# Performance work log

Measured on AMD Instinct MI355X. Metric: run time of the kernel, lower is better.

Reference implementation:

```python
import jax, jax.numpy as jnp
import numpy as np

B, S, D = 4, 4096, 1024
H, F = 16, 256
HD = D // H  # 64


def setup_inputs() -> dict:
    key = jax.random.key(0)
    ks = jax.random.split(key, 10)
    scale = 1.0 / np.sqrt(D)
    x = jax.random.normal(ks[0], (B, S, D), dtype=jnp.float32)
    Wq = jax.random.normal(ks[1], (D, D), dtype=jnp.float32) * scale
    bq = jnp.zeros((D,), dtype=jnp.float32)
    Wk = jax.random.normal(ks[2], (D, D), dtype=jnp.float32) * scale
    bk = jnp.zeros((D,), dtype=jnp.float32)
    Wv = jax.random.normal(ks[3], (D, D), dtype=jnp.float32) * scale
    bv = jnp.zeros((D,), dtype=jnp.float32)
    Wo = jax.random.normal(ks[4], (D, D), dtype=jnp.float32) * scale
    bo = jnp.zeros((D,), dtype=jnp.float32)
    rf = jax.random.normal(ks[5], (H, HD, F), dtype=jnp.float32) / np.sqrt(F)
    return {"x": x, "Wq": Wq, "bq": bq, "Wk": Wk, "bk": bk,
            "Wv": Wv, "bv": bv, "Wo": Wo, "bo": bo, "rf": rf}


def _heads(y):
    # [B,S,D] -> [B,H,S,HD]
    return y.reshape(B, S, H, HD).transpose(0, 2, 1, 3)


def reference(x, Wq, bq, Wk, bk, Wv, bv, Wo, bo, rf):
    q = _heads(x @ Wq.T + bq)
    k = _heads(x @ Wk.T + bk)
    v = _heads(x @ Wv.T + bv)
    # positive feature maps: softplus(random projection)
    q_prime = jax.nn.softplus(jnp.einsum('bhsd,hdf->bhsf', q, rf))
    k_prime = jax.nn.softplus(jnp.einsum('bhsd,hdf->bhsf', k, rf))
    kv = jnp.einsum('bhsf,bhsd->bhfd', k_prime, v)          # [B,H,F,HD]
    k_sum = k_prime.sum(axis=2)                              # [B,H,F]
    qkv = jnp.einsum('bhsf,bhfd->bhsd', q_prime, kv)        # [B,H,S,HD]
    denom = jnp.einsum('bhsf,bhf->bhs', q_prime, k_sum) + 1e-8
    out = qkv / denom[..., None]
    out = out.transpose(0, 2, 1, 3).reshape(B, S, D)
    return out @ Wo.T + bo
```

## Files before the change

kernel.cpp:

```cpp
#include <hip/hip_runtime.h>
#include <hip/hip_bf16.h>
#include <math.h>

#define Bb 4
#define Ss 4096
#define Dd 1024
#define Hh 16
#define Ff 256
#define HDd 64
#define Mm (Bb*Ss)

typedef unsigned int u32;
typedef unsigned short u16;

typedef __attribute__((ext_vector_type(8))) short bf16x8;
typedef __attribute__((ext_vector_type(4))) float f32x4;

__device__ __forceinline__ float bflo(u32 u){ union{u32 i; float f;} c; c.i = u << 16; return c.f; }
__device__ __forceinline__ float bfhi(u32 u){ union{u32 i; float f;} c; c.i = u & 0xffff0000u; return c.f; }
__device__ __forceinline__ u16 f2b(float f){
  union{float f; u32 i;} c; c.f = f;
  u32 x = c.i;
  return (u16)((x + 0x7fffu + ((x >> 16) & 1u)) >> 16);
}
__device__ __forceinline__ u32 pk2(float lo, float hi){
  union { __hip_bfloat162 h; u32 u; } c;
  c.h = __float22bfloat162_rn(make_float2(lo, hi));
  return c.u;
}
__device__ __forceinline__ float sfast(float x){
  return fmaxf(x, 0.f) + __logf(1.f + __expf(-fabsf(x)));
}
__device__ __forceinline__ void gload_lds16(const u16* g, u16* l){
  __builtin_amdgcn_global_load_lds(
      (const __attribute__((address_space(1))) void*)g,
      (__attribute__((address_space(3))) void*)l, 16, 0, 0);
}

__global__ void cvt_bf16(const float* __restrict__ in, u16* __restrict__ out, int n)
{
  int i = (blockIdx.x * 256 + threadIdx.x) * 8;
  if (i >= n) return;
  float4 a = *reinterpret_cast<const float4*>(in + i);
  float4 b = *reinterpret_cast<const float4*>(in + i + 4);
  *reinterpret_cast<uint4*>(out + i) =
      make_uint4(pk2(a.x, a.y), pk2(a.z, a.w), pk2(b.x, b.y), pk2(b.z, b.w));
}

__global__ void cvt_w4(const float* __restrict__ w0, const float* __restrict__ w1,
                       const float* __restrict__ w2, const float* __restrict__ w3,
                       u16* __restrict__ out)
{
  const int y = blockIdx.y;
  const float* in = (y == 0) ? w0 : (y == 1) ? w1 : (y == 2) ? w2 : w3;
  int i = (blockIdx.x * 256 + threadIdx.x) * 8;
  float4 a = *reinterpret_cast<const float4*>(in + i);
  float4 b = *reinterpret_cast<const float4*>(in + i + 4);
  *reinterpret_cast<uint4*>(out + (size_t)y * Dd * Dd + i) =
      make_uint4(pk2(a.x, a.y), pk2(a.z, a.w), pk2(b.x, b.y), pk2(b.z, b.w));
}

__global__ void zero_f32(float* __restrict__ p, int n)
{
  int i = blockIdx.x * 256 + threadIdx.x;
  if (i < n) p[i] = 0.f;
}

template<typename OT, bool BROW>
__global__ __launch_bounds__(256, 2) void mfma_gemm_bt(
    const u16* __restrict__ A, const u16* __restrict__ W,
    const float* __restrict__ bias, OT* __restrict__ C,
    int M, int N, int K)
{
  __shared__ __align__(16) u16 As[128 * 64];
  __shared__ __align__(16) u16 Bs[128 * 64];

  const int tid = threadIdx.x;
  const int wave = tid >> 6, lane = tid & 63;
  const int quad = lane >> 4, lm = lane & 15;
  const int wm = (wave >> 1) * 64, wn = (wave & 1) * 64;
  const int m0 = blockIdx.x * 128, n0 = blockIdx.y * 128;

  int rr[4], cc4[4];
#pragma unroll
  for (int i = 0; i < 4; i++) {
    const int j = wave * 64 + i * 256 + lane;
    rr[i] = j >> 3;
    cc4[i] = (j & 7) ^ (rr[i] & 7);
  }

  f32x4 acc[4][4] = {};

  for (int k0 = 0; k0 < K; k0 += 64) {
#pragma unroll
    for (int i = 0; i < 4; i++) {
      u16* ldsA = &As[(wave * 64 + i * 256) * 8];
      u16* ldsB = &Bs[(wave * 64 + i * 256) * 8];
      gload_lds16(A + (size_t)(m0 + rr[i]) * K + k0 + cc4[i] * 8, ldsA);
      gload_lds16(W + (size_t)(n0 + rr[i]) * K + k0 + cc4[i] * 8, ldsB);
    }
    __syncthreads();

#pragma unroll
    for (int ks2 = 0; ks2 < 2; ks2++) {
      bf16x8 af[4], bf[4];
#pragma unroll
      for (int mi = 0; mi < 4; mi++) {
        const int row = wm + mi * 16 + lm;
        af[mi] = *reinterpret_cast<const bf16x8*>(
            &As[row * 64 + (((ks2 * 4 + quad) ^ (row & 7)) * 8)]);
      }
#pragma unroll
      for (int ni = 0; ni < 4; ni++) {
        const int row = wn + ni * 16 + lm;
        bf[ni] = *reinterpret_cast<const bf16x8*>(
            &Bs[row * 64 + (((ks2 * 4 + quad) ^ (row & 7)) * 8)]);
      }
#pragma unroll
      for (int mi = 0; mi < 4; mi++)
#pragma unroll
        for (int ni = 0; ni < 4; ni++)
          acc[mi][ni] = __builtin_amdgcn_mfma_f32_16x16x32_bf16(af[mi], bf[ni], acc[mi][ni], 0, 0, 0);
    }
    __syncthreads();
  }

#pragma unroll
  for (int mi = 0; mi < 4; mi++)
#pragma unroll
    for (int ni = 0; ni < 4; ni++) {
      const int n = n0 + wn + ni * 16 + lm;
      const float bvn = BROW ? 0.f : bias[n];
      const int mb = m0 + wm + mi * 16 + quad * 4;
      float v[4];
#pragma unroll
      for (int r = 0; r < 4; r++)
        v[r] = acc[mi][ni][r] + (BROW ? bias[mb + r] : bvn);
      if constexpr (sizeof(OT) == 2) {
        const u32 w01 = pk2(v[0], v[1]), w23 = pk2(v[2], v[3]);
        ((u16*)C)[(size_t)(mb + 0) * N + n] = (u16)w01;
        ((u16*)C)[(size_t)(mb + 1) * N + n] = (u16)(w01 >> 16);
        ((u16*)C)[(size_t)(mb + 2) * N + n] = (u16)w23;
        ((u16*)C)[(size_t)(mb + 3) * N + n] = (u16)(w23 >> 16);
      } else {
#pragma unroll
        for (int r = 0; r < 4; r++)
          ((float*)C)[(size_t)(mb + r) * N + n] = v[r];
      }
    }
}

__global__ void rf_transpose(const float* __restrict__ rf, float* __restrict__ rft)
{
  const int h = blockIdx.x, d = blockIdx.y, f = threadIdx.x;
  rft[((size_t)h * Ff + f) * HDd + d] = rf[((size_t)(h * HDd + d)) * Ff + f];
}

#define NSPLIT 16
#define SCHUNKS (Ss / NSPLIT / 64)

__global__ __launch_bounds__(256, 2) void kv_fused(
    const u16* __restrict__ Km, const u16* __restrict__ Vt,
    const float* __restrict__ rft, float* __restrict__ kv, float* __restrict__ ksum)
{
  __shared__ __align__(16) u16 KS[64 * 64];
  __shared__ __align__(16) u16 VS[64 * 64];
  __shared__ __align__(16) u16 PT[4][64 * 64];

  const int bh = blockIdx.x;
  const int b = bh >> 4, h = bh & 15;
  const int s0 = blockIdx.y * (Ss / NSPLIT);
  const int tid = threadIdx.x;
  const int wave = tid >> 6, lane = tid & 63;
  const int quad = lane >> 4, lm = lane & 15;
  const int F0 = wave * 64;

  bf16x8 bfr[4][2];
  {
    const float* rh = rft + (size_t)h * Ff * HDd;
#pragma unroll
    for (int ni = 0; ni < 4; ni++) {
      const float* rrow = rh + (size_t)(F0 + ni * 16 + lm) * HDd;
#pragma unroll
      for (int ks = 0; ks < 2; ks++) {
        float4 a = *reinterpret_cast<const float4*>(rrow + ks * 32 + quad * 8);
        float4 e = *reinterpret_cast<const float4*>(rrow + ks * 32 + quad * 8 + 4);
        union { u32 w[4]; bf16x8 v; } u;
        u.w[0] = pk2(a.x, a.y); u.w[1] = pk2(a.z, a.w);
        u.w[2] = pk2(e.x, e.y); u.w[3] = pk2(e.z, e.w);
        bfr[ni][ks] = u.v;
      }
    }
  }

  const int j0 = wave * 64 + lane, j1 = j0 + 256;
  const int r0 = j0 >> 3, c0 = (j0 & 7) ^ (r0 & 7);
  const int r1 = j1 >> 3, c1 = (j1 & 7) ^ (r1 & 7);

  f32x4 kvacc[4][4] = {};
  float kss[4] = {0.f, 0.f, 0.f, 0.f};

#pragma unroll 1
  for (int ch = 0; ch < SCHUNKS; ch++) {
    const int sc = s0 + ch * 64;
    gload_lds16(Km + (size_t)(b * Ss + sc + r0) * Dd + h * 64 + c0 * 8, &KS[(wave * 64) * 8]);
    gload_lds16(Km + (size_t)(b * Ss + sc + r1) * Dd + h * 64 + c1 * 8, &KS[(wave * 64 + 256) * 8]);
    gload_lds16(Vt + (size_t)(h * 64 + r0) * Mm + b * Ss + sc + c0 * 8, &VS[(wave * 64) * 8]);
    gload_lds16(Vt + (size_t)(h * 64 + r1) * Mm + b * Ss + sc + c1 * 8, &VS[(wave * 64 + 256) * 8]);
    __syncthreads();

#pragma unroll
    for (int mi = 0; mi < 4; mi++) {
      const int row = mi * 16 + lm;
      f32x4 pmi[4] = {};
#pragma unroll
      for (int ks2 = 0; ks2 < 2; ks2++) {
        bf16x8 af = *reinterpret_cast<const bf16x8*>(
            (const char*)KS + row * 128 + (((ks2 * 4 + quad) ^ (row & 7)) * 16));
#pragma unroll
        for (int ni = 0; ni < 4; ni++)
          pmi[ni] = __builtin_amdgcn_mfma_f32_16x16x32_bf16(af, bfr[ni][ks2], pmi[ni], 0, 0, 0);
      }
#pragma unroll
      for (int ni = 0; ni < 4; ni++) {
        float v0 = sfast(pmi[ni][0]);
        float v1 = sfast(pmi[ni][1]);
        float v2 = sfast(pmi[ni][2]);
        float v3 = sfast(pmi[ni][3]);
        kss[ni] += (v0 + v1) + (v2 + v3);
        int frow = ni * 16 + lm;
        int off = (frow * 128 + mi * 32 + quad * 8) ^ ((frow & 7) << 4);
        *reinterpret_cast<uint2*>((char*)&PT[wave][0] + off) =
            make_uint2(pk2(v0, v1), pk2(v2, v3));
      }
    }

#pragma unroll
    for (int ks2 = 0; ks2 < 2; ks2++) {
      bf16x8 a2[4], b2[4];
#pragma unroll
      for (int mi = 0; mi < 4; mi++) {
        int row = mi * 16 + lm;
        a2[mi] = *reinterpret_cast<const bf16x8*>(
            (char*)&PT[wave][0] + row * 128 + (((ks2 * 4 + quad) ^ (row & 7)) * 16));
      }
#pragma unroll
      for (int ni = 0; ni < 4; ni++) {
        int row = ni * 16 + lm;
        b2[ni] = *reinterpret_cast<const bf16x8*>(
            (const char*)VS + row * 128 + (((ks2 * 4 + quad) ^ (row & 7)) * 16));
      }
#pragma unroll
      for (int mi = 0; mi < 4; mi++)
#pragma unroll
        for (int ni = 0; ni < 4; ni++)
          kvacc[mi][ni] = __builtin_amdgcn_mfma_f32_16x16x32_bf16(a2[mi], b2[ni], kvacc[mi][ni], 0, 0, 0);
    }
    __syncthreads();
  }

  float* kvp = kv + (size_t)bh * Ff * HDd;
#pragma unroll
  for (int mi = 0; mi < 4; mi++)
#pragma unroll
    for (int ni = 0; ni < 4; ni++)
#pragma unroll
      for (int rr2 = 0; rr2 < 4; rr2++) {
        int f = F0 + mi * 16 + quad * 4 + rr2;
        int d = ni * 16 + lm;
        atomicAdd(kvp + (size_t)f * HDd + d, kvacc[mi][ni][rr2]);
      }
#pragma unroll
  for (int ni = 0; ni < 4; ni++) {
    float v = kss[ni];
    v += __shfl_xor(v, 16, 64);
    v += __shfl_xor(v, 32, 64);
    if (quad == 0) atomicAdd(ksum + (size_t)bh * Ff + F0 + ni * 16 + lm, v);
  }
}

__global__ void kvt_cvt(const float* __restrict__ kv, u16* __restrict__ kvtb)
{
  const int bh = blockIdx.x;
  const int d = threadIdx.x & 63, fg = threadIdx.x >> 6;
  const float* src = kv + (size_t)bh * Ff * HDd + d;
  u32* dst = reinterpret_cast<u32*>(kvtb + (size_t)bh * HDd * Ff + (size_t)d * Ff + fg * 64);
#pragma unroll
  for (int j = 0; j < 32; j++) {
    float v0 = src[(size_t)(fg * 64 + 2 * j) * HDd];
    float v1 = src[(size_t)(fg * 64 + 2 * j + 1) * HDd];
    dst[j] = pk2(v0, v1);
  }
}

#define ASPLIT 16
#define ACHUNKS (Ss / ASPLIT / 64)

__global__ __launch_bounds__(256, 2) void attn_fused(
    const u16* __restrict__ Qm, const float* __restrict__ rft,
    const u16* __restrict__ kvtb, const float* __restrict__ ksum,
    u16* __restrict__ attnb)
{
  __shared__ __align__(16) u16 P4[4][64 * 64];
  __shared__ __align__(16) float den4[64][4];

  const int bh = blockIdx.x;
  const int b = bh >> 4, h = bh & 15;
  const int s0 = blockIdx.y * (Ss / ASPLIT);
  const int tid = threadIdx.x;
  const int wave = tid >> 6, lane = tid & 63;
  const int quad = lane >> 4, lm = lane & 15;
  const int F0 = wave * 64;

  bf16x8 bfr[4][2];
  {
    const float* rh = rft + (size_t)h * Ff * HDd;
#pragma unroll
    for (int ni = 0; ni < 4; ni++) {
      const float* rrow = rh + (size_t)(F0 + ni * 16 + lm) * HDd;
#pragma unroll
      for (int ks = 0; ks < 2; ks++) {
        float4 a = *reinterpret_cast<const float4*>(rrow + ks * 32 + quad * 8);
        float4 e = *reinterpret_cast<const float4*>(rrow + ks * 32 + quad * 8 + 4);
        union { u32 w[4]; bf16x8 v; } u;
        u.w[0] = pk2(a.x, a.y); u.w[1] = pk2(a.z, a.w);
        u.w[2] = pk2(e.x, e.y); u.w[3] = pk2(e.z, e.w);
        bfr[ni][ks] = u.v;
      }
    }
  }
  bf16x8 b2r[4][2];
  {
    const u16* kb = kvtb + (size_t)bh * HDd * Ff + (size_t)(wave * 16 + lm) * Ff;
#pragma unroll
    for (int fb = 0; fb < 4; fb++)
#pragma unroll
      for (int k2 = 0; k2 < 2; k2++)
        b2r[fb][k2] = *reinterpret_cast<const bf16x8*>(kb + fb * 64 + k2 * 32 + quad * 8);
  }
  float ksv[4];
#pragma unroll
  for (int ni = 0; ni < 4; ni++)
    ksv[ni] = ksum[(size_t)bh * Ff + F0 + ni * 16 + lm];

  const int odd = lm & 1;
  u32 pOffA[4], pOffB[4];
  char* const ptb = (char*)&P4[wave][0];
  {
    const int ra = quad * 4 + (odd ? 2 : 0);
    const int rb = quad * 4 + (odd ? 3 : 1);
#pragma unroll
    for (int ni = 0; ni < 4; ni++) {
      const int fpb = ni * 16 + (lm & ~1);
      const int cc = fpb >> 3, bib = (fpb & 7) * 2;
      pOffA[ni] = ra * 128 + ((cc ^ (ra & 7)) << 4) + bib;
      pOffB[ni] = rb * 128 + ((cc ^ (rb & 7)) << 4) + bib;
    }
  }

  for (int ch = 0; ch < ACHUNKS; ch++) {
    const int sc0 = s0 + ch * 64;

    bf16x8 af[4][2];
#pragma unroll
    for (int mi = 0; mi < 4; mi++) {
      const u16* qrow = Qm + (size_t)(b * Ss + sc0 + mi * 16 + lm) * Dd + h * 64;
#pragma unroll
      for (int ks = 0; ks < 2; ks++)
        af[mi][ks] = *reinterpret_cast<const bf16x8*>(qrow + ks * 32 + quad * 8);
    }
    f32x4 p[4][4] = {};
#pragma unroll
    for (int ks = 0; ks < 2; ks++)
#pragma unroll
      for (int mi = 0; mi < 4; mi++)
#pragma unroll
        for (int ni = 0; ni < 4; ni++)
          p[mi][ni] = __builtin_amdgcn_mfma_f32_16x16x32_bf16(af[mi][ks], bfr[ni][ks], p[mi][ni], 0, 0, 0);

#pragma unroll
    for (int mi = 0; mi < 4; mi++) {
      const int sbase = mi * 16 + quad * 4;
      float dd[4] = {0.f, 0.f, 0.f, 0.f};
#pragma unroll
      for (int ni = 0; ni < 4; ni++) {
        u32 pk01 = pk2(sfast(p[mi][ni][0]), sfast(p[mi][ni][1]));
        u32 pk23 = pk2(sfast(p[mi][ni][2]), sfast(p[mi][ni][3]));
        dd[0] += bflo(pk01) * ksv[ni];
        dd[1] += bfhi(pk01) * ksv[ni];
        dd[2] += bflo(pk23) * ksv[ni];
        dd[3] += bfhi(pk23) * ksv[ni];
        u32 ob01 = (u32)__shfl_xor((int)pk01, 1, 64);
        u32 ob23 = (u32)__shfl_xor((int)pk23, 1, 64);
        u32 s0v = odd ? ob23 : pk01;
        u32 s1v = odd ? pk23 : ob01;
        u32 w_a = __builtin_amdgcn_perm(s1v, s0v, 0x05040100u);
        u32 w_b = __builtin_amdgcn_perm(s1v, s0v, 0x07060302u);
        *reinterpret_cast<u32*>(ptb + pOffA[ni] + mi * 2048) = w_a;
        *reinterpret_cast<u32*>(ptb + pOffB[ni] + mi * 2048) = w_b;
      }
#pragma unroll
      for (int r = 0; r < 4; r++) {
        float v = dd[r];
        v += __shfl_xor(v, 1, 64);
        v += __shfl_xor(v, 2, 64);
        v += __shfl_xor(v, 4, 64);
        v += __shfl_xor(v, 8, 64);
        if (lm == 0) den4[sbase + r][wave] = v;
      }
    }
    __syncthreads();

    f32x4 acc2[4] = {};
#pragma unroll
    for (int fb = 0; fb < 4; fb++)
#pragma unroll
      for (int k2 = 0; k2 < 2; k2++) {
        bf16x8 af2[4];
#pragma unroll
        for (int mi = 0; mi < 4; mi++) {
          int row = mi * 16 + lm;
          af2[mi] = *reinterpret_cast<const bf16x8*>(
              (char*)&P4[fb][0] + row * 128 + (((k2 * 4 + quad) ^ (row & 7)) << 4));
        }
#pragma unroll
        for (int mi = 0; mi < 4; mi++)
          acc2[mi] = __builtin_amdgcn_mfma_f32_16x16x32_bf16(af2[mi], b2r[fb][k2], acc2[mi], 0, 0, 0);
      }

#pragma unroll
    for (int mi = 0; mi < 4; mi++) {
      float o[4];
#pragma unroll
      for (int r = 0; r < 4; r++) {
        const int s = mi * 16 + quad * 4 + r;
        float4 dv = *reinterpret_cast<const float4*>(&den4[s][0]);
        const float inv = 1.f / ((dv.x + dv.y) + (dv.z + dv.w) + 1e-8f);
        o[r] = acc2[mi][r] * inv;
      }
      const u32 w01 = pk2(o[0], o[1]), w23 = pk2(o[2], o[3]);
      const size_t ob = (size_t)(b * Ss + sc0 + mi * 16 + quad * 4) * Dd + h * 64 + wave * 16 + lm;
      attnb[ob]          = (u16)w01;
      attnb[ob + Dd]     = (u16)(w01 >> 16);
      attnb[ob + 2 * Dd] = (u16)w23;
      attnb[ob + 3 * Dd] = (u16)(w23 >> 16);
    }
    __syncthreads();
  }
}

extern "C" void kernel_launch(void* const* d_in, const int* in_sizes, int n_in,
                              void* d_out, int out_size, void* d_ws, size_t ws_size,
                              hipStream_t stream)
{
  const float* x  = (const float*)d_in[0];
  const float* Wq = (const float*)d_in[1];
  const float* bq = (const float*)d_in[2];
  const float* Wk = (const float*)d_in[3];
  const float* bk = (const float*)d_in[4];
  const float* Wv = (const float*)d_in[5];
  const float* bv = (const float*)d_in[6];
  const float* Wo = (const float*)d_in[7];
  const float* bo = (const float*)d_in[8];
  const float* rf = (const float*)d_in[9];

  char* w = (char*)d_ws;
  u16* xb = (u16*)w;        w += (size_t)Mm * Dd * 2;
  u16* q  = (u16*)w;        w += (size_t)Mm * Dd * 2;
  u16* k  = (u16*)w;        w += (size_t)Mm * Dd * 2;
  u16* vt = (u16*)w;        w += (size_t)Mm * Dd * 2;
  u16* wqb = (u16*)w;       w += (size_t)Dd * Dd * 2;
  u16* wkb = (u16*)w;       w += (size_t)Dd * Dd * 2;
  u16* wvb = (u16*)w;       w += (size_t)Dd * Dd * 2;
  u16* wob = (u16*)w;       w += (size_t)Dd * Dd * 2;
  float* kv = (float*)w;    w += (size_t)(Bb * Hh) * Ff * HDd * 4;
  float* ks = (float*)w;    w += (size_t)(Bb * Hh) * Ff * 4;
  float* rft = (float*)w;   w += (size_t)Hh * Ff * HDd * 4;
  u16* kvtb = wqb;

  cvt_bf16<<<(Mm * Dd / 8 + 255) / 256, 256, 0, stream>>>(x, xb, Mm * Dd);
  cvt_w4<<<dim3(Dd * Dd / 8 / 256, 4), 256, 0, stream>>>(Wq, Wk, Wv, Wo, wqb);

  const int nz = (Bb * Hh) * Ff * HDd + (Bb * Hh) * Ff;
  zero_f32<<<(nz + 255) / 256, 256, 0, stream>>>(kv, nz);
  rf_transpose<<<dim3(Hh, HDd), 256, 0, stream>>>(rf, rft);

  const dim3 gg(Mm / 128, Dd / 128);
  mfma_gemm_bt<u16, false><<<gg, 256, 0, stream>>>(xb, wqb, bq, q, Mm, Dd, Dd);
  mfma_gemm_bt<u16, false><<<gg, 256, 0, stream>>>(xb, wkb, bk, k, Mm, Dd, Dd);
  const dim3 gv(Dd / 128, Mm / 128);
  mfma_gemm_bt<u16, true><<<gv, 256, 0, stream>>>(wvb, xb, bv, vt, Dd, Mm, Dd);

  kv_fused<<<dim3(Bb * Hh, NSPLIT), 256, 0, stream>>>(k, vt, rft, kv, ks);

  kvt_cvt<<<Bb * Hh, 256, 0, stream>>>(kv, kvtb);

  attn_fused<<<dim3(Bb * Hh, ASPLIT), 256, 0, stream>>>(q, rft, kvtb, ks, xb);

  mfma_gemm_bt<float, false><<<gg, 256, 0, stream>>>(xb, wob, bo, (float*)d_out, Mm, Dd, Dd);
}
```

Measured before the change: 499.4 us.

## Double-buffer GEMM LDS tiles and restructure attention Q-projection per row block

The bf16 GEMM now keeps two LDS buffers for A and W tiles and prefetches the next K-slice while computing the current one, with explicit vmcnt waits and raw barriers replacing __syncthreads. This is meant to hide global-to-LDS load latency behind MFMA work. LDS use doubles to 64 KB per block, which may limit the two-blocks-per-CU target. Separately, the attention kernel computes the Q feature projection one 16-row block at a time instead of holding all 16 accumulators, lowering register pressure.

New measurement: 492.9 us. About the same (-1.3%).

```diff
diff --git a/kernel.cpp b/kernel.cpp
--- a/kernel.cpp
+++ b/kernel.cpp
@@ -72,8 +72,8 @@
     const float* __restrict__ bias, OT* __restrict__ C,
     int M, int N, int K)
 {
-  __shared__ __align__(16) u16 As[128 * 64];
-  __shared__ __align__(16) u16 Bs[128 * 64];
+  __shared__ __align__(16) u16 As[2][128 * 64];
+  __shared__ __align__(16) u16 Bs[2][128 * 64];
 
   const int tid = threadIdx.x;
   const int wave = tid >> 6, lane = tid & 63;
@@ -91,16 +91,34 @@
 
   f32x4 acc[4][4] = {};
 
-  for (int k0 = 0; k0 < K; k0 += 64) {
-#pragma unroll
-    for (int i = 0; i < 4; i++) {
-      u16* ldsA = &As[(wave * 64 + i * 256) * 8];
-      u16* ldsB = &Bs[(wave * 64 + i * 256) * 8];
-      gload_lds16(A + (size_t)(m0 + rr[i]) * K + k0 + cc4[i] * 8, ldsA);
-      gload_lds16(W + (size_t)(n0 + rr[i]) * K + k0 + cc4[i] * 8, ldsB);
-    }
-    __syncthreads();
-
+#pragma unroll
+  for (int i = 0; i < 4; i++) {
+    gload_lds16(A + (size_t)(m0 + rr[i]) * K + cc4[i] * 8, &As[0][(wave * 64 + i * 256) * 8]);
+    gload_lds16(W + (size_t)(n0 + rr[i]) * K + cc4[i] * 8, &Bs[0][(wave * 64 + i * 256) * 8]);
+  }
+
+  const int NIT = K >> 6;
+#pragma unroll 1
+  for (int it = 0; it < NIT; it++) {
+    const int cur = it & 1;
+    if (it + 1 < NIT) {
+      const int k1 = (it + 1) * 64;
+#pragma unroll
+      for (int i = 0; i < 4; i++) {
+        gload_lds16(A + (size_t)(m0 + rr[i]) * K + k1 + cc4[i] * 8,
+                    &As[cur ^ 1][(wave * 64 + i * 256) * 8]);
+        gload_lds16(W + (size_t)(n0 + rr[i]) * K + k1 + cc4[i] * 8,
+                    &Bs[cur ^ 1][(wave * 64 + i * 256) * 8]);
+      }
+      asm volatile("s_waitcnt vmcnt(8)" ::: "memory");
+    } else {
+      asm volatile("s_waitcnt vmcnt(0)" ::: "memory");
+    }
+    __builtin_amdgcn_s_barrier();
+    __builtin_amdgcn_sched_barrier(0);
+
+    const u16* Ac = &As[cur][0];
+    const u16* Bc = &Bs[cur][0];
 #pragma unroll
     for (int ks2 = 0; ks2 < 2; ks2++) {
       bf16x8 af[4], bf[4];
@@ -108,13 +126,13 @@
       for (int mi = 0; mi < 4; mi++) {
         const int row = wm + mi * 16 + lm;
         af[mi] = *reinterpret_cast<const bf16x8*>(
-            &As[row * 64 + (((ks2 * 4 + quad) ^ (row & 7)) * 8)]);
+            &Ac[row * 64 + (((ks2 * 4 + quad) ^ (row & 7)) * 8)]);
       }
 #pragma unroll
       for (int ni = 0; ni < 4; ni++) {
         const int row = wn + ni * 16 + lm;
         bf[ni] = *reinterpret_cast<const bf16x8*>(
-            &Bs[row * 64 + (((ks2 * 4 + quad) ^ (row & 7)) * 8)]);
+            &Bc[row * 64 + (((ks2 * 4 + quad) ^ (row & 7)) * 8)]);
       }
 #pragma unroll
       for (int mi = 0; mi < 4; mi++)
@@ -122,7 +140,8 @@
         for (int ni = 0; ni < 4; ni++)
           acc[mi][ni] = __builtin_amdgcn_mfma_f32_16x16x32_bf16(af[mi], bf[ni], acc[mi][ni], 0, 0, 0);
     }
-    __syncthreads();
+    __builtin_amdgcn_sched_barrier(0);
+    __builtin_amdgcn_s_barrier();
   }
 
 #pragma unroll
@@ -361,31 +380,25 @@
   for (int ch = 0; ch < ACHUNKS; ch++) {
     const int sc0 = s0 + ch * 64;
 
-    bf16x8 af[4][2];
 #pragma unroll
     for (int mi = 0; mi < 4; mi++) {
       const u16* qrow = Qm + (size_t)(b * Ss + sc0 + mi * 16 + lm) * Dd + h * 64;
-#pragma unroll
-      for (int ks = 0; ks < 2; ks++)
-        af[mi][ks] = *reinterpret_cast<const bf16x8*>(qrow + ks * 32 + quad * 8);
-    }
-    f32x4 p[4][4] = {};
-#pragma unroll
-    for (int ks = 0; ks < 2; ks++)
-#pragma unroll
-      for (int mi = 0; mi < 4; mi++)
-#pragma unroll
-        for (int ni = 0; ni < 4; ni++)
-          p[mi][ni] = __builtin_amdgcn_mfma_f32_16x16x32_bf16(af[mi][ks], bfr[ni][ks], p[mi][ni], 0, 0, 0);
-
-#pragma unroll
-    for (int mi = 0; mi < 4; mi++) {
+      const bf16x8 a0 = *reinterpret_cast<const bf16x8*>(qrow + quad * 8);
+      const bf16x8 a1 = *reinterpret_cast<const bf16x8*>(qrow + 32 + quad * 8);
+      f32x4 pmi[4] = {};
+#pragma unroll
+      for (int ni = 0; ni < 4; ni++)
+        pmi[ni] = __builtin_amdgcn_mfma_f32_16x16x32_bf16(a0, bfr[ni][0], pmi[ni], 0, 0, 0);
+#pragma unroll
+      for (int ni = 0; ni < 4; ni++)
+        pmi[ni] = __builtin_amdgcn_mfma_f32_16x16x32_bf16(a1, bfr[ni][1], pmi[ni], 0, 0, 0);
+
       const int sbase = mi * 16 + quad * 4;
       float dd[4] = {0.f, 0.f, 0.f, 0.f};
 #pragma unroll
       for (int ni = 0; ni < 4; ni++) {
-        u32 pk01 = pk2(sfast(p[mi][ni][0]), sfast(p[mi][ni][1]));
-        u32 pk23 = pk2(sfast(p[mi][ni][2]), sfast(p[mi][ni][3]));
+        u32 pk01 = pk2(sfast(pmi[ni][0]), sfast(pmi[ni][1]));
+        u32 pk23 = pk2(sfast(pmi[ni][2]), sfast(pmi[ni][3]));
         dd[0] += bflo(pk01) * ksv[ni];
         dd[1] += bfhi(pk01) * ksv[ni];
         dd[2] += bflo(pk23) * ksv[ni];
```
